# Performance work log

Measured on AMD Instinct MI355X. Metric: run time of the kernel, lower is better.

## Reference

```python
import jax, jax.numpy as jnp
import numpy as np

N_NODES = 50000
N_EDGES = 500000
NEG_SLOPE = 0.2


def gat_layer(x, src, dst, W, a_src, a_dst, b, n):
    """PyG-style GATConv (add_self_loops=True, concat=True, eval mode).
    x: [N, F_in], W: [F_in, H*C], a_src/a_dst: [H, C], b: [H*C]."""
    H, C = a_src.shape
    h = (x @ W).reshape(-1, H, C)              # [N, H, C]
    loops = jnp.arange(n, dtype=src.dtype)
    s = jnp.concatenate([src, loops])          # self-loops appended
    d = jnp.concatenate([dst, loops])
    alpha_src = jnp.einsum('nhc,hc->nh', h, a_src)   # [N, H]
    alpha_dst = jnp.einsum('nhc,hc->nh', h, a_dst)
    e = jax.nn.leaky_relu(alpha_src[s] + alpha_dst[d], NEG_SLOPE)  # [E+N, H]
    m = jax.ops.segment_max(e, d, num_segments=n)    # segment softmax over dst
    w = jnp.exp(e - m[d])
    denom = jax.ops.segment_sum(w, d, num_segments=n)
    attn = w / (denom[d] + 1e-16)                    # [E+N, H]
    msg = h[s] * attn[:, :, None]                    # [E+N, H, C]
    out = jax.ops.segment_sum(msg, d, num_segments=n)  # [N, H, C]
    return out.reshape(n, H * C) + b


def setup_inputs() -> dict:
    key = jax.random.key(0)
    ks = jax.random.split(key, 20)
    F_in, Hd, Hh = 128, 64, 4
    g = lambda k, shp, fan: jax.random.normal(k, shp, jnp.float32) * (1.0 / np.sqrt(fan))
    inp = {
        'x': jax.random.normal(ks[0], (N_NODES, F_in), jnp.float32),
        'edge_index': jax.random.randint(ks[1], (2, N_EDGES), 0, N_NODES, jnp.int32),
        'W1': g(ks[2], (F_in, Hh * Hd), F_in),
        'a1s': g(ks[3], (Hh, Hd), Hd), 'a1d': g(ks[4], (Hh, Hd), Hd),
        'b1': jnp.zeros((Hh * Hd,), jnp.float32),
        'W2': g(ks[5], (Hh * Hd, Hh * Hd), Hh * Hd),
        'a2s': g(ks[6], (Hh, Hd), Hd), 'a2d': g(ks[7], (Hh, Hd), Hd),
        'b2': jnp.zeros((Hh * Hd,), jnp.float32),
        'W3': g(ks[8], (Hh * Hd, Hd), Hh * Hd),
        'a3s': g(ks[9], (1, Hd), Hd), 'a3d': g(ks[10], (1, Hd), Hd),
        'b3': jnp.zeros((Hd,), jnp.float32),
        'cW1': g(ks[11], (Hd, Hd // 2), Hd), 'cb1': jnp.zeros((Hd // 2,), jnp.float32),
        'cW2': g(ks[12], (Hd // 2, 2), Hd // 2), 'cb2': jnp.zeros((2,), jnp.float32),
    }
    return inp


def reference(x, edge_index, W1, a1s, a1d, b1, W2, a2s, a2d, b2,
              W3, a3s, a3d, b3, cW1, cb1, cW2, cb2):
    n = x.shape[0]
    src, dst = edge_index[0], edge_index[1]
    h = jax.nn.elu(gat_layer(x, src, dst, W1, a1s, a1d, b1, n))
    h = jax.nn.elu(gat_layer(h, src, dst, W2, a2s, a2d, b2, n))
    h = jax.nn.relu(gat_layer(h, src, dst, W3, a3s, a3d, b3, n))
    h = jax.nn.relu(h @ cW1 + cb1)
    logits = h @ cW2 + cb2
    return jax.nn.log_softmax(logits, axis=1)
```

## Files before the change

### kernel.cpp

```cpp
#include <hip/hip_runtime.h>
#include <hip/hip_fp16.h>

#define LRELU(v) ((v) > 0.f ? (v) : 0.2f * (v))

typedef _Float16 f16x8 __attribute__((ext_vector_type(8)));
typedef float f32x4 __attribute__((ext_vector_type(4)));

__device__ __forceinline__ f16x8 f16x8_zero() {
    f16x8 v;
#pragma unroll
    for (int j = 0; j < 8; ++j) v[j] = (_Float16)0.f;
    return v;
}

__global__ __launch_bounds__(256) void hist_kernel(const int* __restrict__ dst,
                                                   int* __restrict__ cnt, int E) {
    int e = blockIdx.x * 256 + threadIdx.x;
    if (e < E) atomicAdd(&cnt[dst[e]], 1);
}

__global__ __launch_bounds__(256) void scan_blk(const int* __restrict__ cnt,
                                                int* __restrict__ offv,
                                                int* __restrict__ bsum, int N) {
    __shared__ int sh[256];
    const int t = threadIdx.x;
    const int base = blockIdx.x * 1024 + t * 4;
    int v0 = (base + 0 < N) ? cnt[base + 0] : 0;
    int v1 = (base + 1 < N) ? cnt[base + 1] : 0;
    int v2 = (base + 2 < N) ? cnt[base + 2] : 0;
    int v3 = (base + 3 < N) ? cnt[base + 3] : 0;
    const int T = v0 + v1 + v2 + v3;
    sh[t] = T;
    __syncthreads();
    for (int o = 1; o < 256; o <<= 1) {
        int x = (t >= o) ? sh[t - o] : 0;
        __syncthreads();
        sh[t] += x;
        __syncthreads();
    }
    const int excl = sh[t] - T;
    if (t == 255) bsum[blockIdx.x] = sh[255];
    if (base + 0 < N) offv[base + 0] = excl;
    if (base + 1 < N) offv[base + 1] = excl + v0;
    if (base + 2 < N) offv[base + 2] = excl + v0 + v1;
    if (base + 3 < N) offv[base + 3] = excl + v0 + v1 + v2;
}

__global__ __launch_bounds__(64) void scan_top(int* __restrict__ bsum,
                                               int* __restrict__ offv,
                                               int NB, int N) {
    const int t = threadIdx.x;
    const int v = (t < NB) ? bsum[t] : 0;
    int incl = v;
#pragma unroll
    for (int o = 1; o < 64; o <<= 1) {
        int x = __shfl_up(incl, o);
        if (t >= o) incl += x;
    }
    if (t < NB) bsum[t] = incl - v;
    if (t == NB - 1) offv[N] = incl;
}

__global__ __launch_bounds__(256) void scan_add(int* __restrict__ offv,
                                                const int* __restrict__ bsum, int N) {
    const int base = blockIdx.x * 1024 + threadIdx.x * 4;
    const int add = bsum[blockIdx.x];
#pragma unroll
    for (int i = 0; i < 4; ++i)
        if (base + i < N) offv[base + i] += add;
}

__global__ __launch_bounds__(256) void fill_kernel(const int* __restrict__ dst,
                                                   const int* __restrict__ srcv,
                                                   const int* __restrict__ offv,
                                                   int* __restrict__ cur,
                                                   int* __restrict__ csrsrc, int E) {
    int e = blockIdx.x * 256 + threadIdx.x;
    if (e < E) {
        int d = dst[e];
        int p = atomicAdd(&cur[d], 1);
        csrsrc[offv[d] + p] = srcv[e];
    }
}

__global__ __launch_bounds__(256) void prep_w16(const float* __restrict__ W,
                                                _Float16* __restrict__ wt,
                                                int K, int Nn) {
    int idx = blockIdx.x * 256 + threadIdx.x;
    if (idx < K * Nn) {
        int k = idx / Nn, nn2 = idx - k * Nn;
        wt[(size_t)nn2 * K + k] = (_Float16)W[idx];
    }
}

__global__ __launch_bounds__(256) void cvt_f16(const float* __restrict__ in,
                                               _Float16* __restrict__ out, int n4) {
    int i = blockIdx.x * 256 + threadIdx.x;
    if (i < n4) {
        float4 v = *(const float4*)(in + (size_t)i * 4);
        _Float16 o[4] = {(_Float16)v.x, (_Float16)v.y, (_Float16)v.z, (_Float16)v.w};
        *(float2*)(out + (size_t)i * 4) = *(float2*)o;
    }
}

template <int WM, int WN, int K, int H>
__global__ __launch_bounds__(WM * WN * 64) void gemm_f16_fused(
    const _Float16* __restrict__ A, const _Float16* __restrict__ Wt,
    const float* __restrict__ a_s, const float* __restrict__ a_d,
    _Float16* __restrict__ hout, float* __restrict__ als,
    float* __restrict__ ald, int M, int Nn) {
    constexpr int BM = WM * 64;
    constexpr int T = WM * WN * 64;
    constexpr int CHUNKS = BM * 16;
    __shared__ f16x8 Atile[BM * 16];
    const int t = threadIdx.x;
    const int lane = t & 63;
    const int wv = t >> 6;
    const int wm = wv / WN, wn = wv % WN;
    const int m0 = blockIdx.x * BM;
    const int n0 = blockIdx.y * (WN * 64);
    const int l15 = lane & 15, lg = lane >> 4;

    f32x4 acc[4][4];
    const f32x4 zz = {0.f, 0.f, 0.f, 0.f};
#pragma unroll
    for (int mi = 0; mi < 4; ++mi)
#pragma unroll
        for (int ni = 0; ni < 4; ++ni) acc[mi][ni] = zz;

    for (int kc = 0; kc < K; kc += 128) {
        __syncthreads();
#pragma unroll
        for (int i = 0; i < CHUNKS / T; ++i) {
            const int c = i * T + t;
            const int row = c >> 4, cc = c & 15;
            const int gr = m0 + row;
            f16x8 v = (gr < M) ? *(const f16x8*)(A + (size_t)gr * K + kc + cc * 8)
                               : f16x8_zero();
            Atile[(row * 16 + cc) ^ (row & 7)] = v;
        }
        __syncthreads();
#pragma unroll
        for (int ks = 0; ks < 4; ++ks) {
            f16x8 af[4], bf[4];
#pragma unroll
            for (int mi = 0; mi < 4; ++mi) {
                const int row = wm * 64 + mi * 16 + l15;
                af[mi] = Atile[(row * 16 + ks * 4 + lg) ^ (row & 7)];
            }
#pragma unroll
            for (int ni = 0; ni < 4; ++ni) {
                const int col = n0 + wn * 64 + ni * 16 + l15;
                bf[ni] = *(const f16x8*)(Wt + (size_t)col * K + kc + ks * 32 + lg * 8);
            }
#pragma unroll
            for (int mi = 0; mi < 4; ++mi)
#pragma unroll
                for (int ni = 0; ni < 4; ++ni)
                    acc[mi][ni] = __builtin_amdgcn_mfma_f32_16x16x32_f16(
                        af[mi], bf[ni], acc[mi][ni], 0, 0, 0);
        }
    }
    const int head = (n0 + wn * 64) >> 6;
    float a4s[4], a4d[4];
#pragma unroll
    for (int ni = 0; ni < 4; ++ni) {
        a4s[ni] = a_s[head * 64 + ni * 16 + l15];
        a4d[ni] = a_d[head * 64 + ni * 16 + l15];
    }
#pragma unroll
    for (int mi = 0; mi < 4; ++mi)
#pragma unroll
        for (int j = 0; j < 4; ++j) {
            const int r = m0 + wm * 64 + mi * 16 + lg * 4 + j;
            if (r < M) {
                float s1 = 0.f, s2 = 0.f;
#pragma unroll
                for (int ni = 0; ni < 4; ++ni) {
                    const float v = acc[mi][ni][j];
                    s1 += v * a4s[ni];
                    s2 += v * a4d[ni];
                    hout[(size_t)r * Nn + n0 + wn * 64 + ni * 16 + l15] = (_Float16)v;
                }
#pragma unroll
                for (int o = 8; o; o >>= 1) {
                    s1 += __shfl_xor(s1, o);
                    s2 += __shfl_xor(s2, o);
                }
                if (l15 == 0) {
                    als[(size_t)r * H + head] = s1;
                    ald[(size_t)r * H + head] = s2;
                }
            }
        }
}

__device__ __forceinline__ float sel4(float4 v, int h) {
    float r = v.x;
    r = (h == 1) ? v.y : r;
    r = (h == 2) ? v.z : r;
    r = (h == 3) ? v.w : r;
    return r;
}

__global__ __launch_bounds__(64) void gat_agg_h4(
    const __half* __restrict__ hhf, const float4* __restrict__ als4,
    const float4* __restrict__ ald4, const int* __restrict__ csrsrc,
    const int* __restrict__ offv, const float* __restrict__ bias,
    __half* __restrict__ outh) {
    const int n = blockIdx.x;
    const int t = threadIdx.x;
    const int hh = t >> 4;
    __shared__ int sid[64];
    __shared__ float4 wsh[64];
    const int start = offv[n];
    const int deg = offv[n + 1] - start;
    const float4 ad = ald4[n];
    const float4 asf = als4[n];
    float4 m4;
    m4.x = LRELU(asf.x + ad.x);
    m4.y = LRELU(asf.y + ad.y);
    m4.z = LRELU(asf.z + ad.z);
    m4.w = LRELU(asf.w + ad.w);
    float acc[4];
    {
        float2 raw = *(const float2*)(hhf + (size_t)n * 256 + t * 4);
        __half2 h0 = *(__half2*)&raw.x;
        __half2 h1 = *(__half2*)&raw.y;
        float2 a0 = __half22float2(h0), a1 = __half22float2(h1);
        acc[0] = a0.x; acc[1] = a0.y; acc[2] = a1.x; acc[3] = a1.y;
    }
    float dsum = 1.f;

    for (int base = 0; base < deg; base += 64) {
        const int nb = deg - base;
        const bool valid = t < nb;
        int s = 0;
        float4 e;
        if (valid) {
            s = csrsrc[start + base + t];
            const float4 av = als4[s];
            e.x = LRELU(av.x + ad.x);
            e.y = LRELU(av.y + ad.y);
            e.z = LRELU(av.z + ad.z);
            e.w = LRELU(av.w + ad.w);
        } else {
            e.x = e.y = e.z = e.w = -1e30f;
        }
        float4 cm = e;
#pragma unroll
        for (int o = 32; o; o >>= 1) {
            cm.x = fmaxf(cm.x, __shfl_xor(cm.x, o));
            cm.y = fmaxf(cm.y, __shfl_xor(cm.y, o));
            cm.z = fmaxf(cm.z, __shfl_xor(cm.z, o));
            cm.w = fmaxf(cm.w, __shfl_xor(cm.w, o));
        }
        float4 nm;
        nm.x = fmaxf(m4.x, cm.x);
        nm.y = fmaxf(m4.y, cm.y);
        nm.z = fmaxf(m4.z, cm.z);
        nm.w = fmaxf(m4.w, cm.w);
        const float sc = __expf(sel4(m4, hh) - sel4(nm, hh));
        acc[0] *= sc; acc[1] *= sc; acc[2] *= sc; acc[3] *= sc;
        dsum *= sc;
        m4 = nm;
        float4 w;
        w.x = __expf(e.x - nm.x);
        w.y = __expf(e.y - nm.y);
        w.z = __expf(e.z - nm.z);
        w.w = __expf(e.w - nm.w);
        float4 ws = w;
#pragma unroll
        for (int o = 32; o; o >>= 1) {
            ws.x += __shfl_xor(ws.x, o);
            ws.y += __shfl_xor(ws.y, o);
            ws.z += __shfl_xor(ws.z, o);
            ws.w += __shfl_xor(ws.w, o);
        }
        dsum += sel4(ws, hh);
        __syncthreads();
        sid[t] = s;
        wsh[t] = w;
        __syncthreads();
        const int nbc = min(nb, 64);
        const float* wflat = (const float*)wsh;
        for (int i = 0; i < nbc; ++i) {
            const int s2 = sid[i];
            const float wvv = wflat[i * 4 + hh];
            float2 raw = *(const float2*)(hhf + (size_t)s2 * 256 + t * 4);
            __half2 h0 = *(__half2*)&raw.x;
            __half2 h1 = *(__half2*)&raw.y;
            float2 a0 = __half22float2(h0), a1 = __half22float2(h1);
            acc[0] += a0.x * wvv; acc[1] += a0.y * wvv;
            acc[2] += a1.x * wvv; acc[3] += a1.y * wvv;
        }
    }
    const float inv = 1.f / (dsum + 1e-16f);
    const float4 bv = *(const float4*)(bias + t * 4);
    float4 o4;
    o4.x = acc[0] * inv + bv.x;
    o4.y = acc[1] * inv + bv.y;
    o4.z = acc[2] * inv + bv.z;
    o4.w = acc[3] * inv + bv.w;
    o4.x = (o4.x > 0.f) ? o4.x : (__expf(o4.x) - 1.f);
    o4.y = (o4.y > 0.f) ? o4.y : (__expf(o4.y) - 1.f);
    o4.z = (o4.z > 0.f) ? o4.z : (__expf(o4.z) - 1.f);
    o4.w = (o4.w > 0.f) ? o4.w : (__expf(o4.w) - 1.f);
    __half2 p0 = __floats2half2_rn(o4.x, o4.y);
    __half2 p1 = __floats2half2_rn(o4.z, o4.w);
    float2 st;
    *(__half2*)&st.x = p0;
    *(__half2*)&st.y = p1;
    *(float2*)(outh + (size_t)n * 256 + t * 4) = st;
}

__global__ __launch_bounds__(64) void gat_agg_h1(
    const __half* __restrict__ hhf, const float* __restrict__ als,
    const float* __restrict__ ald, const int* __restrict__ csrsrc,
    const int* __restrict__ offv, const float* __restrict__ bias,
    float* __restrict__ outp) {
    const int n = blockIdx.x;
    const int t = threadIdx.x;
    __shared__ int sid[64];
    __shared__ float wsh[64];
    const int start = offv[n];
    const int deg = offv[n + 1] - start;
    const float ad = ald[n];
    float m = LRELU(als[n] + ad);
    float acc = __half2float(hhf[(size_t)n * 64 + t]);
    float dsum = 1.f;

    for (int base = 0; base < deg; base += 64) {
        const int nb = deg - base;
        const bool valid = t < nb;
        int s = 0;
        float e = -1e30f;
        if (valid) {
            s = csrsrc[start + base + t];
            e = LRELU(als[s] + ad);
        }
        float cm = e;
#pragma unroll
        for (int o = 32; o; o >>= 1) cm = fmaxf(cm, __shfl_xor(cm, o));
        const float nm = fmaxf(m, cm);
        const float sc = __expf(m - nm);
        acc *= sc;
        dsum *= sc;
        m = nm;
        const float w = __expf(e - nm);
        float ws = w;
#pragma unroll
        for (int o = 32; o; o >>= 1) ws += __shfl_xor(ws, o);
        dsum += ws;
        __syncthreads();
        sid[t] = s;
        wsh[t] = w;
        __syncthreads();
        const int nbc = min(nb, 64);
        for (int i = 0; i < nbc; ++i)
            acc += __half2float(hhf[(size_t)sid[i] * 64 + t]) * wsh[i];
    }
    float val = acc / (dsum + 1e-16f) + bias[t];
    val = fmaxf(val, 0.f);
    outp[(size_t)n * 64 + t] = val;
}

__global__ __launch_bounds__(64) void classifier_kernel(
    const float* __restrict__ h3, const float* __restrict__ cW1,
    const float* __restrict__ cb1, const float* __restrict__ cW2,
    const float* __restrict__ cb2, float* __restrict__ outp) {
    const int n = blockIdx.x;
    const int t = threadIdx.x;
    __shared__ float xs[64];
    __shared__ float hid[32];
    __shared__ float lg[2];
    xs[t] = h3[(size_t)n * 64 + t];
    __syncthreads();
    if (t < 32) {
        float s = cb1[t];
#pragma unroll
        for (int c = 0; c < 64; ++c) s += xs[c] * cW1[c * 32 + t];
        hid[t] = fmaxf(s, 0.f);
    }
    __syncthreads();
    if (t < 2) {
        float s = cb2[t];
#pragma unroll
        for (int j = 0; j < 32; ++j) s += hid[j] * cW2[j * 2 + t];
        lg[t] = s;
    }
    __syncthreads();
    if (t == 0) {
        float a = lg[0], b = lg[1];
        float mm = fmaxf(a, b);
        float lse = mm + logf(__expf(a - mm) + __expf(b - mm));
        outp[(size_t)n * 2 + 0] = a - lse;
        outp[(size_t)n * 2 + 1] = b - lse;
    }
}

extern "C" void kernel_launch(void* const* d_in, const int* in_sizes, int n_in,
                              void* d_out, int out_size, void* d_ws, size_t ws_size,
                              hipStream_t stream) {
    const float* x   = (const float*)d_in[0];
    const int*   ei  = (const int*)d_in[1];
    const float* W1  = (const float*)d_in[2];
    const float* a1s = (const float*)d_in[3];
    const float* a1d = (const float*)d_in[4];
    const float* b1  = (const float*)d_in[5];
    const float* W2  = (const float*)d_in[6];
    const float* a2s = (const float*)d_in[7];
    const float* a2d = (const float*)d_in[8];
    const float* b2  = (const float*)d_in[9];
    const float* W3  = (const float*)d_in[10];
    const float* a3s = (const float*)d_in[11];
    const float* a3d = (const float*)d_in[12];
    const float* b3  = (const float*)d_in[13];
    const float* cW1 = (const float*)d_in[14];
    const float* cb1 = (const float*)d_in[15];
    const float* cW2 = (const float*)d_in[16];
    const float* cb2 = (const float*)d_in[17];

    const int N = in_sizes[0] / 128;
    const int E = in_sizes[1] / 2;
    const int* srcv = ei;
    const int* dstv = ei + E;

    char* p = (char*)d_ws;
    _Float16* slotA = (_Float16*)p; p += (size_t)N * 256 * 2;
    _Float16* slotB = (_Float16*)p; p += (size_t)N * 256 * 2;
    _Float16* slotC = (_Float16*)p; p += (size_t)N * 128 * 2;
    float* slotD = (float*)p; p += (size_t)N * 64 * 4;
    float* als = (float*)p; p += (size_t)N * 4 * 4;
    float* ald = (float*)p; p += (size_t)N * 4 * 4;
    int* cnt = (int*)p; p += (size_t)N * 4;
    int* offv = (int*)p; p += (size_t)(N + 4) * 4;
    int* csr = (int*)p; p += (size_t)E * 4;
    _Float16* Wt1 = (_Float16*)p; p += (size_t)128 * 256 * 2;
    _Float16* Wt2 = (_Float16*)p; p += (size_t)256 * 256 * 2;
    _Float16* Wt3 = (_Float16*)p; p += (size_t)256 * 64 * 2;
    int* bsum = (int*)p;

    prep_w16<<<(128 * 256 + 255) / 256, 256, 0, stream>>>(W1, Wt1, 128, 256);
    prep_w16<<<(256 * 256 + 255) / 256, 256, 0, stream>>>(W2, Wt2, 256, 256);
    prep_w16<<<(256 * 64 + 255) / 256, 256, 0, stream>>>(W3, Wt3, 256, 64);
    cvt_f16<<<(N * 128 / 4 + 255) / 256, 256, 0, stream>>>(x, slotC, N * 128 / 4);

    const int NB = (N + 1023) / 1024;
    hipMemsetAsync(cnt, 0, (size_t)N * sizeof(int), stream);
    hist_kernel<<<(E + 255) / 256, 256, 0, stream>>>(dstv, cnt, E);
    scan_blk<<<NB, 256, 0, stream>>>(cnt, offv, bsum, N);
    scan_top<<<1, 64, 0, stream>>>(bsum, offv, NB, N);
    scan_add<<<NB, 256, 0, stream>>>(offv, bsum, N);
    hipMemsetAsync(cnt, 0, (size_t)N * sizeof(int), stream);
    fill_kernel<<<(E + 255) / 256, 256, 0, stream>>>(dstv, srcv, offv, cnt, csr, E);

    const int MB128 = (N + 127) / 128;
    const int MB256 = (N + 255) / 256;

    gemm_f16_fused<2, 4, 128, 4><<<dim3(MB128, 1), 512, 0, stream>>>(
        slotC, Wt1, a1s, a1d, slotA, als, ald, N, 256);
    gat_agg_h4<<<N, 64, 0, stream>>>((const __half*)slotA, (const float4*)als,
                                     (const float4*)ald, csr, offv, b1,
                                     (__half*)slotB);

    gemm_f16_fused<2, 4, 256, 4><<<dim3(MB128, 1), 512, 0, stream>>>(
        slotB, Wt2, a2s, a2d, slotA, als, ald, N, 256);
    gat_agg_h4<<<N, 64, 0, stream>>>((const __half*)slotA, (const float4*)als,
                                     (const float4*)ald, csr, offv, b2,
                                     (__half*)slotB);

    gemm_f16_fused<4, 1, 256, 1><<<dim3(MB256, 1), 256, 0, stream>>>(
        slotB, Wt3, a3s, a3d, slotC, als, ald, N, 64);
    gat_agg_h1<<<N, 64, 0, stream>>>((const __half*)slotC, als, ald, csr, offv,
                                     b3, slotD);

    classifier_kernel<<<N, 64, 0, stream>>>(slotD, cW1, cb1, cW2, cb2, (float*)d_out);
}
```

Before: 310.9 us.

## Drop online-softmax max tracking in GAT aggregation and fuse classifier into last layer

The aggregation kernels no longer track a running max or rescale, and no longer do wavefront shuffle reductions. They compute exp(leaky_relu(e)) directly and accumulate the denominator in the gather loop. The last GAT aggregation kernel now also runs the classifier MLP and log-softmax, which removes a kernel launch and the fp32 intermediate buffer. Without max subtraction, large attention logits could overflow, so correctness depends on the logits staying within exp range.

```diff
diff --git a/kernel.cpp b/kernel.cpp
--- a/kernel.cpp
+++ b/kernel.cpp
@@ -217,70 +217,38 @@
     const int deg = offv[n + 1] - start;
     const float4 ad = ald4[n];
     const float4 asf = als4[n];
-    float4 m4;
-    m4.x = LRELU(asf.x + ad.x);
-    m4.y = LRELU(asf.y + ad.y);
-    m4.z = LRELU(asf.z + ad.z);
-    m4.w = LRELU(asf.w + ad.w);
+    float4 ws4;
+    ws4.x = __expf(LRELU(asf.x + ad.x));
+    ws4.y = __expf(LRELU(asf.y + ad.y));
+    ws4.z = __expf(LRELU(asf.z + ad.z));
+    ws4.w = __expf(LRELU(asf.w + ad.w));
+    const float wself = sel4(ws4, hh);
     float acc[4];
     {
         float2 raw = *(const float2*)(hhf + (size_t)n * 256 + t * 4);
         __half2 h0 = *(__half2*)&raw.x;
         __half2 h1 = *(__half2*)&raw.y;
         float2 a0 = __half22float2(h0), a1 = __half22float2(h1);
-        acc[0] = a0.x; acc[1] = a0.y; acc[2] = a1.x; acc[3] = a1.y;
-    }
-    float dsum = 1.f;
+        acc[0] = a0.x * wself; acc[1] = a0.y * wself;
+        acc[2] = a1.x * wself; acc[3] = a1.y * wself;
+    }
+    float dsum = wself;
 
     for (int base = 0; base < deg; base += 64) {
         const int nb = deg - base;
-        const bool valid = t < nb;
         int s = 0;
-        float4 e;
-        if (valid) {
+        float4 w4 = {0.f, 0.f, 0.f, 0.f};
+        if (t < nb) {
             s = csrsrc[start + base + t];
             const float4 av = als4[s];
-            e.x = LRELU(av.x + ad.x);
-            e.y = LRELU(av.y + ad.y);
-            e.z = LRELU(av.z + ad.z);
-            e.w = LRELU(av.w + ad.w);
-        } else {
-            e.x = e.y = e.z = e.w = -1e30f;
-        }
-        float4 cm = e;
-#pragma unroll
-        for (int o = 32; o; o >>= 1) {
-            cm.x = fmaxf(cm.x, __shfl_xor(cm.x, o));
-            cm.y = fmaxf(cm.y, __shfl_xor(cm.y, o));
-            cm.z = fmaxf(cm.z, __shfl_xor(cm.z, o));
-            cm.w = fmaxf(cm.w, __shfl_xor(cm.w, o));
-        }
-        float4 nm;
-        nm.x = fmaxf(m4.x, cm.x);
-        nm.y = fmaxf(m4.y, cm.y);
-        nm.z = fmaxf(m4.z, cm.z);
-        nm.w = fmaxf(m4.w, cm.w);
-        const float sc = __expf(sel4(m4, hh) - sel4(nm, hh));
-        acc[0] *= sc; acc[1] *= sc; acc[2] *= sc; acc[3] *= sc;
-        dsum *= sc;
-        m4 = nm;
-        float4 w;
-        w.x = __expf(e.x - nm.x);
-        w.y = __expf(e.y - nm.y);
-        w.z = __expf(e.z - nm.z);
-        w.w = __expf(e.w - nm.w);
-        float4 ws = w;
-#pragma unroll
-        for (int o = 32; o; o >>= 1) {
-            ws.x += __shfl_xor(ws.x, o);
-            ws.y += __shfl_xor(ws.y, o);
-            ws.z += __shfl_xor(ws.z, o);
-            ws.w += __shfl_xor(ws.w, o);
-        }
-        dsum += sel4(ws, hh);
+            w4.x = __expf(LRELU(av.x + ad.x));
+            w4.y = __expf(LRELU(av.y + ad.y));
+            w4.z = __expf(LRELU(av.z + ad.z));
+            w4.w = __expf(LRELU(av.w + ad.w));
+        }
         __syncthreads();
         sid[t] = s;
-        wsh[t] = w;
+        wsh[t] = w4;
         __syncthreads();
         const int nbc = min(nb, 64);
         const float* wflat = (const float*)wsh;
@@ -291,6 +259,7 @@
             __half2 h0 = *(__half2*)&raw.x;
             __half2 h1 = *(__half2*)&raw.y;
             float2 a0 = __half22float2(h0), a1 = __half22float2(h1);
+            dsum += wvv;
             acc[0] += a0.x * wvv; acc[1] += a0.y * wvv;
             acc[2] += a1.x * wvv; acc[3] += a1.y * wvv;
         }
@@ -314,67 +283,50 @@
     *(float2*)(outh + (size_t)n * 256 + t * 4) = st;
 }
 
-__global__ __launch_bounds__(64) void gat_agg_h1(
+__global__ __launch_bounds__(64) void gat_agg_h1_cls(
     const __half* __restrict__ hhf, const float* __restrict__ als,
     const float* __restrict__ ald, const int* __restrict__ csrsrc,
     const int* __restrict__ offv, const float* __restrict__ bias,
+    const float* __restrict__ cW1, const float* __restrict__ cb1,
+    const float* __restrict__ cW2, const float* __restrict__ cb2,
     float* __restrict__ outp) {
     const int n = blockIdx.x;
     const int t = threadIdx.x;
     __shared__ int sid[64];
     __shared__ float wsh[64];
+    __shared__ float xs[64];
+    __shared__ float hid[32];
+    __shared__ float lg[2];
     const int start = offv[n];
     const int deg = offv[n + 1] - start;
     const float ad = ald[n];
-    float m = LRELU(als[n] + ad);
-    float acc = __half2float(hhf[(size_t)n * 64 + t]);
-    float dsum = 1.f;
+    const float wself = __expf(LRELU(als[n] + ad));
+    float acc = __half2float(hhf[(size_t)n * 64 + t]) * wself;
+    float dsum = wself;
 
     for (int base = 0; base < deg; base += 64) {
         const int nb = deg - base;
-        const bool valid = t < nb;
         int s = 0;
-        float e = -1e30f;
-        if (valid) {
+        float w = 0.f;
+        if (t < nb) {
             s = csrsrc[start + base + t];
-            e = LRELU(als[s] + ad);
-        }
-        float cm = e;
-#pragma unroll
-        for (int o = 32; o; o >>= 1) cm = fmaxf(cm, __shfl_xor(cm, o));
-        const float nm = fmaxf(m, cm);
-        const float sc = __expf(m - nm);
-        acc *= sc;
-        dsum *= sc;
-        m = nm;
-        const float w = __expf(e - nm);
-        float ws = w;
-#pragma unroll
-        for (int o = 32; o; o >>= 1) ws += __shfl_xor(ws, o);
-        dsum += ws;
+            w = __expf(LRELU(als[s] + ad));
+        }
         __syncthreads();
         sid[t] = s;
         wsh[t] = w;
         __syncthreads();
         const int nbc = min(nb, 64);
-        for (int i = 0; i < nbc; ++i)
-            acc += __half2float(hhf[(size_t)sid[i] * 64 + t]) * wsh[i];
+        for (int i = 0; i < nbc; ++i) {
+            const float wvv = wsh[i];
+            dsum += wvv;
+            acc += __half2float(hhf[(size_t)sid[i] * 64 + t]) * wvv;
+        }
     }
     float val = acc / (dsum + 1e-16f) + bias[t];
     val = fmaxf(val, 0.f);
-    outp[(size_t)n * 64 + t] = val;
-}
-
-__global__ __launch_bounds__(64) void classifier_kernel(
-    const float* __restrict__ h3, const float* __restrict__ cW1,
-    const float* __restrict__ cb1, const float* __restrict__ cW2,
-    const float* __restrict__ cb2, float* __restrict__ outp) {
-    const int n = blockIdx.x;
-    const int t = threadIdx.x;
-    __shared__ float xs[64];
-    __shared__ float hid[32];
-    __shared__ float lg[2];
-    xs[t] = h3[(size_t)n * 64 + t];
+    __syncthreads();
+    xs[t] = val;
     __syncthreads();
     if (t < 32) {
         float s = cb1[t];
@@ -430,7 +382,6 @@
     _Float16* slotA = (_Float16*)p; p += (size_t)N * 256 * 2;
     _Float16* slotB = (_Float16*)p; p += (size_t)N * 256 * 2;
     _Float16* slotC = (_Float16*)p; p += (size_t)N * 128 * 2;
-    float* slotD = (float*)p; p += (size_t)N * 64 * 4;
     float* als = (float*)p; p += (size_t)N * 4 * 4;
     float* ald = (float*)p; p += (size_t)N * 4 * 4;
     int* cnt = (int*)p; p += (size_t)N * 4;
@@ -471,9 +422,7 @@
                                      (__half*)slotB);
 
     gemm_f16_fused<4, 1, 256, 1><<<dim3(MB256, 1), 256, 0, stream>>>(
-        slotB, Wt3, a3s, a3d, slotC, als, ald, N, 64);
-    gat_agg_h1<<<N, 64, 0, stream>>>((const __half*)slotC, als, ald, csr, offv,
-                                     b3, slotD);
-
-    classifier_kernel<<<N, 64, 0, stream>>>(slotD, cW1, cb1, cW2, cb2, (float*)d_out);
-}
+        slotB, Wt3, a3s, a3d, slotA, als, ald, N, 64);
+    gat_agg_h1_cls<<<N, 64, 0, stream>>>((const __half*)slotA, als, ald, csr, offv,
+                                         b3, cW1, cb1, cW2, cb2, (float*)d_out);
+}
```

Result: faster. 296.0 us (-4.8%).
